# Kernel optimization log

Hardware: AMD Instinct MI355X
Metric: run time of the kernel (lower is better)

Reference implementation:

```python
import jax, jax.numpy as jnp
import numpy as np

H = 512          # hidden_dim
T = 20           # output_seq_len
EPS = 1e-5


def _ln(x, g, b):
    m = jnp.mean(x, axis=-1, keepdims=True)
    v = jnp.mean((x - m) ** 2, axis=-1, keepdims=True)
    return (x - m) * jax.lax.rsqrt(v + EPS) * g + b


def setup_inputs() -> dict:
    key = jax.random.key(0)
    ks = jax.random.split(key, 20)
    N, LD, PD = 65536, 128, 32
    s = 0.02
    return {
        "z_q": jax.random.normal(ks[0], (N, LD), jnp.float32),
        "f_prior": jax.random.normal(ks[1], (N, PD), jnp.float32),
        # init_mlp: Linear(160 -> 1024) -> LN -> GELU -> Linear(1024 -> 512) -> Tanh
        "W1": jax.random.normal(ks[2], (LD + PD, 2 * H), jnp.float32) * s,
        "b1": jnp.zeros((2 * H,), jnp.float32),
        "g1": jnp.ones((2 * H,), jnp.float32),
        "be1": jnp.zeros((2 * H,), jnp.float32),
        "W2": jax.random.normal(ks[3], (2 * H, H), jnp.float32) * s,
        "b2": jnp.zeros((H,), jnp.float32),
        # start token (output_dim = 1)
        "start_token": jax.random.normal(ks[4], (1,), jnp.float32) * 0.1,
        # GRU, input_size=1, hidden_size=H, gates stacked [r, z, n] (torch layout)
        "W_ih": jax.random.normal(ks[5], (3 * H, 1), jnp.float32) * s,
        "W_hh": jax.random.normal(ks[6], (3 * H, H), jnp.float32) * s,
        "b_ih": jnp.zeros((3 * H,), jnp.float32),
        "b_hh": jnp.zeros((3 * H,), jnp.float32),
        # output_mlp: Linear(H -> H//2) -> LN -> GELU -> Linear(H//2 -> 1)
        "Wo1": jax.random.normal(ks[7], (H, H // 2), jnp.float32) * s,
        "bo1": jnp.zeros((H // 2,), jnp.float32),
        "go": jnp.ones((H // 2,), jnp.float32),
        "beo": jnp.zeros((H // 2,), jnp.float32),
        "Wo2": jax.random.normal(ks[8], (H // 2, 1), jnp.float32) * s,
        "bo2": jnp.zeros((1,), jnp.float32),
    }


def reference(z_q, f_prior, W1, b1, g1, be1, W2, b2, start_token,
              W_ih, W_hh, b_ih, b_hh, Wo1, bo1, go, beo, Wo2, bo2):
    N = z_q.shape[0]
    # init_mlp -> h_0 (dropout is identity at eval)
    combined = jnp.concatenate([z_q, f_prior], axis=1)          # (N, LD+PD)
    h = jnp.tanh(jax.nn.gelu(_ln(combined @ W1 + b1, g1, be1), approximate=False) @ W2 + b2)  # (N, H)

    x0 = jnp.broadcast_to(start_token[None, :], (N, 1))          # (N, 1)

    def step(carry, _):
        h, x = carry
        gi = x @ W_ih.T + b_ih                                   # (N, 3H)
        gh = h @ W_hh.T + b_hh                                   # (N, 3H)
        r = jax.nn.sigmoid(gi[:, :H] + gh[:, :H])
        z = jax.nn.sigmoid(gi[:, H:2 * H] + gh[:, H:2 * H])
        n = jnp.tanh(gi[:, 2 * H:] + r * gh[:, 2 * H:])
        h_new = (1.0 - z) * n + z * h
        y = jax.nn.gelu(_ln(h_new @ Wo1 + bo1, go, beo), approximate=False) @ Wo2 + bo2  # (N, 1)
        return (h_new, y), y

    _, ys = jax.lax.scan(step, (h, x0), None, length=T)          # (T, N, 1)
    preds = jnp.transpose(ys[..., 0], (1, 0))                    # (N, T), output_dim==1 squeeze
    return preds
```

## Files before the change

kernel.cpp:

```cpp
#include <hip/hip_runtime.h>
#include <math.h>


typedef _Float16 f16;
typedef _Float16 f16x4 __attribute__((ext_vector_type(4)));
typedef _Float16 f16x8 __attribute__((ext_vector_type(8)));
typedef float f32x4 __attribute__((ext_vector_type(4)));

#define TSTEPS 20

__device__ __forceinline__ float sigm(float v) { return 1.0f / (1.0f + __expf(-v)); }
__device__ __forceinline__ float tanh_s(float v) {
  float e = __expf(-2.0f * fabsf(v));
  float r = (1.0f - e) / (1.0f + e);
  return copysignf(r, v);
}
__device__ __forceinline__ float gelu_e(float v) {
  return 0.5f * v * (1.0f + erff(v * 0.70710678118654752f));
}
__device__ __forceinline__ void st4(float* d, float4 v) {
  d[0] = v.x; d[1] = v.y; d[2] = v.z; d[3] = v.w;
}

__device__ __forceinline__ int haddr(int buf, int m, int k) {
  return buf + m * 1024 + ((k * 2) ^ ((m & 7) << 4));
}
__device__ __forceinline__ int taddr(int m, int c) {
  return m * 2048 + ((c * 2) ^ ((m & 7) << 4));
}

__global__ void cvt_weights(const float* __restrict__ W1, const float* __restrict__ W2,
                            const float* __restrict__ Whh, const float* __restrict__ Wo1,
                            f16* __restrict__ w1t, f16* __restrict__ w2t,
                            f16* __restrict__ whh, f16* __restrict__ wo1t) {
  int i = blockIdx.x * 256 + threadIdx.x;
  if (i < 163840) { int n = i / 160; int k = i - n * 160; w1t[i] = (f16)W1[k * 1024 + n]; return; }
  i -= 163840;
  if (i < 524288) { int n = i >> 10; int k = i & 1023; w2t[i] = (f16)W2[k * 512 + n]; return; }
  i -= 524288;
  if (i < 786432) { whh[i] = (f16)Whh[i]; return; }
  i -= 786432;
  if (i < 131072) { int o = i >> 9; int k = i & 511; wo1t[i] = (f16)Wo1[k * 256 + o]; return; }
}

__global__ __launch_bounds__(512) __attribute__((amdgpu_waves_per_eu(2, 2)))
void gru_main(
    const float* __restrict__ zq, const float* __restrict__ fpr,
    const float* __restrict__ b1, const float* __restrict__ g1, const float* __restrict__ be1,
    const float* __restrict__ b2, const float* __restrict__ stok,
    const float* __restrict__ Wih, const float* __restrict__ bih, const float* __restrict__ bhh,
    const float* __restrict__ bo1, const float* __restrict__ go, const float* __restrict__ beo,
    const float* __restrict__ Wo2, const float* __restrict__ bo2,
    const f16* __restrict__ w1t, const f16* __restrict__ w2t,
    const f16* __restrict__ whh, const f16* __restrict__ wo1t,
    float* __restrict__ out) {
  __shared__ __align__(16) unsigned char sm[131072];
  __shared__ float sm_stat[64 * 9 * 2];
  __shared__ float sm_yp[64 * 9];
  __shared__ float sm_x[64];

  const int tid = threadIdx.x;
  const int w = tid >> 6;
  const int lane = tid & 63;
  const int l16 = lane & 15;
  const int l4 = lane >> 4;
  const int R0 = blockIdx.x * 64;

  if (tid < 64) sm_x[tid] = stok[0];

  #pragma unroll 1
  for (int p = 0; p < 4; ++p) {
    f32x4 acc[4][2];
    #pragma unroll
    for (int mt = 0; mt < 4; ++mt)
      #pragma unroll
      for (int jh = 0; jh < 2; ++jh) acc[mt][jh] = (f32x4){0.f, 0.f, 0.f, 0.f};
    #pragma unroll
    for (int kf = 0; kf < 5; ++kf) {
      const int k0 = kf * 32 + l4 * 8;
      f16x8 B[4];
      #pragma unroll
      for (int mt = 0; mt < 4; ++mt) {
        const int gm = R0 + mt * 16 + l16;
        const float* src = (kf < 4) ? (zq + gm * 128 + k0) : (fpr + gm * 32 + (k0 - 128));
        float4 v0 = *(const float4*)src;
        float4 v1 = *(const float4*)(src + 4);
        f16x8 b;
        b[0] = (f16)v0.x; b[1] = (f16)v0.y; b[2] = (f16)v0.z; b[3] = (f16)v0.w;
        b[4] = (f16)v1.x; b[5] = (f16)v1.y; b[6] = (f16)v1.z; b[7] = (f16)v1.w;
        B[mt] = b;
      }
      f16x8 A[2];
      #pragma unroll
      for (int jh = 0; jh < 2; ++jh)
        A[jh] = *(const f16x8*)(w1t + (w * 128 + (p * 2 + jh) * 16 + l16) * 160 + k0);
      #pragma unroll
      for (int mt = 0; mt < 4; ++mt)
        #pragma unroll
        for (int jh = 0; jh < 2; ++jh)
          acc[mt][jh] = __builtin_amdgcn_mfma_f32_16x16x32_f16(A[jh], B[mt], acc[mt][jh], 0, 0, 0);
    }
    #pragma unroll
    for (int jh = 0; jh < 2; ++jh) {
      const int jq = w * 128 + (p * 2 + jh) * 16 + l4 * 4;
      const float4 bb = *(const float4*)(b1 + jq);
      float bbv[4]; st4(bbv, bb);
      #pragma unroll
      for (int mt = 0; mt < 4; ++mt) {
        const int m = mt * 16 + l16;
        f16x4 v;
        #pragma unroll
        for (int r = 0; r < 4; ++r) v[r] = (f16)(acc[mt][jh][r] + bbv[r]);
        *(f16x4*)(sm + taddr(m, jq)) = v;
      }
    }
  }
  __syncthreads();
  {
    const int m = lane;
    float s = 0.f, ss = 0.f;
    #pragma unroll 4
    for (int cb = 0; cb < 16; ++cb) {
      const int c = w * 128 + cb * 8;
      f16x8 v = *(const f16x8*)(sm + taddr(m, c));
      #pragma unroll
      for (int i = 0; i < 8; ++i) { float f = (float)v[i]; s += f; ss += f * f; }
    }
    sm_stat[(m * 9 + w) * 2] = s;
    sm_stat[(m * 9 + w) * 2 + 1] = ss;
    __syncthreads();
    s = 0.f; ss = 0.f;
    #pragma unroll
    for (int i = 0; i < 8; ++i) { s += sm_stat[(m * 9 + i) * 2]; ss += sm_stat[(m * 9 + i) * 2 + 1]; }
    const float mean = s * (1.f / 1024.f);
    const float rstd = rsqrtf(ss * (1.f / 1024.f) - mean * mean + 1e-5f);
    #pragma unroll 2
    for (int cb = 0; cb < 16; ++cb) {
      const int c = w * 128 + cb * 8;
      f16x8 v = *(const f16x8*)(sm + taddr(m, c));
      float4 ga = *(const float4*)(g1 + c);
      float4 gb = *(const float4*)(g1 + c + 4);
      float4 ba = *(const float4*)(be1 + c);
      float4 bb = *(const float4*)(be1 + c + 4);
      float gs[8] = {ga.x, ga.y, ga.z, ga.w, gb.x, gb.y, gb.z, gb.w};
      float bs[8] = {ba.x, ba.y, ba.z, ba.w, bb.x, bb.y, bb.z, bb.w};
      f16x8 o;
      #pragma unroll
      for (int i = 0; i < 8; ++i)
        o[i] = (f16)gelu_e(((float)v[i] - mean) * rstd * gs[i] + bs[i]);
      *(f16x8*)(sm + taddr(m, c)) = o;
    }
  }
  __syncthreads();
  f16x4 hold[2][4][2];
  #pragma unroll
  for (int p = 0; p < 2; ++p) {
    f32x4 acc[4][2];
    #pragma unroll
    for (int mt = 0; mt < 4; ++mt)
      #pragma unroll
      for (int jh = 0; jh < 2; ++jh) acc[mt][jh] = (f32x4){0.f, 0.f, 0.f, 0.f};
    #pragma unroll 4
    for (int kf = 0; kf < 32; ++kf) {
      const int k0 = kf * 32 + l4 * 8;
      f16x8 B[4];
      #pragma unroll
      for (int mt = 0; mt < 4; ++mt)
        B[mt] = *(const f16x8*)(sm + taddr(mt * 16 + l16, k0));
      f16x8 A[2];
      #pragma unroll
      for (int jh = 0; jh < 2; ++jh)
        A[jh] = *(const f16x8*)(w2t + (w * 64 + (p * 2 + jh) * 16 + l16) * 1024 + k0);
      #pragma unroll
      for (int mt = 0; mt < 4; ++mt)
        #pragma unroll
        for (int jh = 0; jh < 2; ++jh)
          acc[mt][jh] = __builtin_amdgcn_mfma_f32_16x16x32_f16(A[jh], B[mt], acc[mt][jh], 0, 0, 0);
    }
    #pragma unroll
    for (int jh = 0; jh < 2; ++jh) {
      const int jq = w * 64 + (p * 2 + jh) * 16 + l4 * 4;
      const float4 bb = *(const float4*)(b2 + jq);
      float bbv[4]; st4(bbv, bb);
      #pragma unroll
      for (int mt = 0; mt < 4; ++mt) {
        f16x4 v;
        #pragma unroll
        for (int r = 0; r < 4; ++r) v[r] = (f16)tanh_s(acc[mt][jh][r] + bbv[r]);
        hold[p][mt][jh] = v;
      }
    }
  }
  __syncthreads();
  #pragma unroll
  for (int p = 0; p < 2; ++p)
    #pragma unroll
    for (int jh = 0; jh < 2; ++jh) {
      const int jq = w * 64 + (p * 2 + jh) * 16 + l4 * 4;
      #pragma unroll
      for (int mt = 0; mt < 4; ++mt) {
        const int m = mt * 16 + l16;
        *(f16x4*)(sm + haddr(0, m, jq)) = hold[p][mt][jh];
      }
    }
  __syncthreads();

  #pragma unroll 1
  for (int t = 0; t < TSTEPS; ++t) {
    const int cur = (t & 1) << 16;
    const int nxt = cur ^ 65536;
    #pragma unroll 1
    for (int p = 0; p < 2; ++p) {
      f32x4 acc[4][3][2];
      #pragma unroll
      for (int mt = 0; mt < 4; ++mt)
        #pragma unroll
        for (int g = 0; g < 3; ++g)
          #pragma unroll
          for (int jh = 0; jh < 2; ++jh) acc[mt][g][jh] = (f32x4){0.f, 0.f, 0.f, 0.f};
      #pragma unroll 4
      for (int kf = 0; kf < 16; ++kf) {
        const int k0 = kf * 32 + l4 * 8;
        f16x8 B[4];
        #pragma unroll
        for (int mt = 0; mt < 4; ++mt)
          B[mt] = *(const f16x8*)(sm + haddr(cur, mt * 16 + l16, k0));
        f16x8 A[3][2];
        #pragma unroll
        for (int g = 0; g < 3; ++g)
          #pragma unroll
          for (int jh = 0; jh < 2; ++jh)
            A[g][jh] = *(const f16x8*)(whh + (g * 512 + w * 64 + (p * 2 + jh) * 16 + l16) * 512 + k0);
        #pragma unroll
        for (int mt = 0; mt < 4; ++mt)
          #pragma unroll
          for (int g = 0; g < 3; ++g)
            #pragma unroll
            for (int jh = 0; jh < 2; ++jh)
              acc[mt][g][jh] = __builtin_amdgcn_mfma_f32_16x16x32_f16(A[g][jh], B[mt], acc[mt][g][jh], 0, 0, 0);
      }
      #pragma unroll
      for (int jh = 0; jh < 2; ++jh) {
        const int jq = w * 64 + (p * 2 + jh) * 16 + l4 * 4;
        float wr[4], wz[4], wn[4], br[4], bz[4], bn[4], cr[4], cz[4], cn[4];
        st4(wr, *(const float4*)(Wih + jq));
        st4(wz, *(const float4*)(Wih + 512 + jq));
        st4(wn, *(const float4*)(Wih + 1024 + jq));
        st4(br, *(const float4*)(bih + jq));
        st4(bz, *(const float4*)(bih + 512 + jq));
        st4(bn, *(const float4*)(bih + 1024 + jq));
        st4(cr, *(const float4*)(bhh + jq));
        st4(cz, *(const float4*)(bhh + 512 + jq));
        st4(cn, *(const float4*)(bhh + 1024 + jq));
        #pragma unroll
        for (int mt = 0; mt < 4; ++mt) {
          const int m = mt * 16 + l16;
          const float x = sm_x[m];
          const int hoff = m * 1024 + ((jq * 2) ^ ((m & 7) << 4));
          const f16x4 ho = *(const f16x4*)(sm + cur + hoff);
          f16x4 hn;
          #pragma unroll
          for (int r = 0; r < 4; ++r) {
            const float gr = sigm(x * wr[r] + br[r] + acc[mt][0][jh][r] + cr[r]);
            const float gz = sigm(x * wz[r] + bz[r] + acc[mt][1][jh][r] + cz[r]);
            const float gn = tanh_s(x * wn[r] + bn[r] + gr * (acc[mt][2][jh][r] + cn[r]));
            hn[r] = (f16)((1.f - gz) * gn + gz * (float)ho[r]);
          }
          *(f16x4*)(sm + nxt + hoff) = hn;
        }
      }
    }
    __syncthreads();
    {
      f32x4 a2[4][2];
      #pragma unroll
      for (int mt = 0; mt < 4; ++mt)
        #pragma unroll
        for (int jt = 0; jt < 2; ++jt) a2[mt][jt] = (f32x4){0.f, 0.f, 0.f, 0.f};
      #pragma unroll 4
      for (int kf = 0; kf < 16; ++kf) {
        const int k0 = kf * 32 + l4 * 8;
        f16x8 B[4];
        #pragma unroll
        for (int mt = 0; mt < 4; ++mt)
          B[mt] = *(const f16x8*)(sm + haddr(nxt, mt * 16 + l16, k0));
        f16x8 A[2];
        #pragma unroll
        for (int jt = 0; jt < 2; ++jt)
          A[jt] = *(const f16x8*)(wo1t + (w * 32 + jt * 16 + l16) * 512 + k0);
        #pragma unroll
        for (int mt = 0; mt < 4; ++mt)
          #pragma unroll
          for (int jt = 0; jt < 2; ++jt)
            a2[mt][jt] = __builtin_amdgcn_mfma_f32_16x16x32_f16(A[jt], B[mt], a2[mt][jt], 0, 0, 0);
      }
      float vv[4][2][4];
      float bo1v[2][4];
      #pragma unroll
      for (int jt = 0; jt < 2; ++jt)
        st4(bo1v[jt], *(const float4*)(bo1 + w * 32 + jt * 16 + l4 * 4));
      float sA[4], sB[4];
      #pragma unroll
      for (int mt = 0; mt < 4; ++mt) {
        float s = 0.f, ss = 0.f;
        #pragma unroll
        for (int jt = 0; jt < 2; ++jt)
          #pragma unroll
          for (int r = 0; r < 4; ++r) {
            const float v = a2[mt][jt][r] + bo1v[jt][r];
            vv[mt][jt][r] = v; s += v; ss += v * v;
          }
        s += __shfl_xor(s, 16); ss += __shfl_xor(ss, 16);
        s += __shfl_xor(s, 32); ss += __shfl_xor(ss, 32);
        sA[mt] = s; sB[mt] = ss;
      }
      if (l4 == 0) {
        #pragma unroll
        for (int mt = 0; mt < 4; ++mt) {
          const int m = mt * 16 + l16;
          sm_stat[(m * 9 + w) * 2] = sA[mt];
          sm_stat[(m * 9 + w) * 2 + 1] = sB[mt];
        }
      }
      __syncthreads();
      float gov[2][4], bev[2][4], wv[2][4];
      #pragma unroll
      for (int jt = 0; jt < 2; ++jt) {
        const int jb = w * 32 + jt * 16 + l4 * 4;
        st4(gov[jt], *(const float4*)(go + jb));
        st4(bev[jt], *(const float4*)(beo + jb));
        st4(wv[jt], *(const float4*)(Wo2 + jb));
      }
      float yp[4];
      #pragma unroll
      for (int mt = 0; mt < 4; ++mt) {
        const int m = mt * 16 + l16;
        float s = 0.f, ss = 0.f;
        #pragma unroll
        for (int i = 0; i < 8; ++i) {
          s += sm_stat[(m * 9 + i) * 2];
          ss += sm_stat[(m * 9 + i) * 2 + 1];
        }
        const float mean = s * (1.f / 256.f);
        const float rstd = rsqrtf(ss * (1.f / 256.f) - mean * mean + 1e-5f);
        float y = 0.f;
        #pragma unroll
        for (int jt = 0; jt < 2; ++jt)
          #pragma unroll
          for (int r = 0; r < 4; ++r)
            y += gelu_e((vv[mt][jt][r] - mean) * rstd * gov[jt][r] + bev[jt][r]) * wv[jt][r];
        y += __shfl_xor(y, 16);
        y += __shfl_xor(y, 32);
        yp[mt] = y;
      }
      if (l4 == 0) {
        #pragma unroll
        for (int mt = 0; mt < 4; ++mt)
          sm_yp[(mt * 16 + l16) * 9 + w] = yp[mt];
      }
      __syncthreads();
      if (w == 0 && l4 == 0) {
        #pragma unroll
        for (int mt = 0; mt < 4; ++mt) {
          const int m = mt * 16 + l16;
          float y = bo2[0];
          #pragma unroll
          for (int i = 0; i < 8; ++i) y += sm_yp[m * 9 + i];
          sm_x[m] = y;
          out[(R0 + m) * 20 + t] = y;
        }
      }
      __syncthreads();
    }
  }
}

extern "C" void kernel_launch(void* const* d_in, const int* in_sizes, int n_in,
                              void* d_out, int out_size, void* d_ws, size_t ws_size,
                              hipStream_t stream) {
  const float* zq   = (const float*)d_in[0];
  const float* fpr  = (const float*)d_in[1];
  const float* W1   = (const float*)d_in[2];
  const float* b1   = (const float*)d_in[3];
  const float* g1   = (const float*)d_in[4];
  const float* be1  = (const float*)d_in[5];
  const float* W2   = (const float*)d_in[6];
  const float* b2   = (const float*)d_in[7];
  const float* stok = (const float*)d_in[8];
  const float* Wih  = (const float*)d_in[9];
  const float* Whh  = (const float*)d_in[10];
  const float* bih  = (const float*)d_in[11];
  const float* bhh  = (const float*)d_in[12];
  const float* Wo1  = (const float*)d_in[13];
  const float* bo1  = (const float*)d_in[14];
  const float* go   = (const float*)d_in[15];
  const float* beo  = (const float*)d_in[16];
  const float* Wo2  = (const float*)d_in[17];
  const float* bo2  = (const float*)d_in[18];

  char* ws = (char*)d_ws;
  f16* w1t  = (f16*)(ws + 0);
  f16* w2t  = (f16*)(ws + 327680);
  f16* whh  = (f16*)(ws + 1376256);
  f16* wo1t = (f16*)(ws + 2949120);

  cvt_weights<<<6272, 256, 0, stream>>>(W1, W2, Whh, Wo1, w1t, w2t, whh, wo1t);

  const int N = in_sizes[0] / 128;
  gru_main<<<N / 64, 512, 0, stream>>>(zq, fpr, b1, g1, be1, b2, stok, Wih, bih, bhh,
                                       bo1, go, beo, Wo2, bo2, w1t, w2t, whh, wo1t,
                                       (float*)d_out);
}
```

Before: 5.299 ms.

## Halve LDS and registers to allow two blocks per CU

LDS drops from 128KB to 64KB. The hidden-state double buffer becomes a single buffer, with new h values held in registers until a barrier and then written back. The init MLP now runs in two 32-row halves so its pre-activation tile fits the smaller buffer. Per-iteration accumulator sets are smaller, waves_per_eu rises to 4, and the final per-row output sum is computed redundantly by every wave, which removes one barrier and the sm_x buffer. This aims for higher occupancy so latency is hidden better, at the cost of an extra barrier per step and possible register spills.

```diff
diff --git a/kernel.cpp b/kernel.cpp
--- a/kernel.cpp
+++ b/kernel.cpp
@@ -22,8 +22,8 @@
   d[0] = v.x; d[1] = v.y; d[2] = v.z; d[3] = v.w;
 }
 
-__device__ __forceinline__ int haddr(int buf, int m, int k) {
-  return buf + m * 1024 + ((k * 2) ^ ((m & 7) << 4));
+__device__ __forceinline__ int haddr(int m, int k) {
+  return m * 1024 + ((k * 2) ^ ((m & 7) << 4));
 }
 __device__ __forceinline__ int taddr(int m, int c) {
   return m * 2048 + ((c * 2) ^ ((m & 7) << 4));
@@ -43,7 +43,7 @@
   if (i < 131072) { int o = i >> 9; int k = i & 511; wo1t[i] = (f16)Wo1[k * 256 + o]; return; }
 }
 
-__global__ __launch_bounds__(512) __attribute__((amdgpu_waves_per_eu(2, 2)))
+__global__ __launch_bounds__(512) __attribute__((amdgpu_waves_per_eu(4)))
 void gru_main(
     const float* __restrict__ zq, const float* __restrict__ fpr,
     const float* __restrict__ b1, const float* __restrict__ g1, const float* __restrict__ be1,
@@ -54,10 +54,9 @@
     const f16* __restrict__ w1t, const f16* __restrict__ w2t,
     const f16* __restrict__ whh, const f16* __restrict__ wo1t,
     float* __restrict__ out) {
-  __shared__ __align__(16) unsigned char sm[131072];
+  __shared__ __align__(16) unsigned char sm[65536];
   __shared__ float sm_stat[64 * 9 * 2];
   __shared__ float sm_yp[64 * 9];
-  __shared__ float sm_x[64];
 
   const int tid = threadIdx.x;
   const int w = tid >> 6;
@@ -66,209 +65,207 @@
   const int l4 = lane >> 4;
   const int R0 = blockIdx.x * 64;
 
-  if (tid < 64) sm_x[tid] = stok[0];
+  const float bo2v = bo2[0];
+  float x4[4];
+  {
+    const float s0 = stok[0];
+    #pragma unroll
+    for (int mt = 0; mt < 4; ++mt) x4[mt] = s0;
+  }
+
+  f16x4 h0h[2][2][2][2];
 
   #pragma unroll 1
-  for (int p = 0; p < 4; ++p) {
-    f32x4 acc[4][2];
+  for (int hh = 0; hh < 2; ++hh) {
+    const int RH = R0 + hh * 32;
+    #pragma unroll 1
+    for (int q = 0; q < 4; ++q) {
+      f32x4 acc[2][2];
+      #pragma unroll
+      for (int mt = 0; mt < 2; ++mt)
+        #pragma unroll
+        for (int jh = 0; jh < 2; ++jh) acc[mt][jh] = (f32x4){0.f, 0.f, 0.f, 0.f};
+      #pragma unroll
+      for (int kf = 0; kf < 5; ++kf) {
+        const int k0 = kf * 32 + l4 * 8;
+        f16x8 B[2];
+        #pragma unroll
+        for (int mt = 0; mt < 2; ++mt) {
+          const int gm = RH + mt * 16 + l16;
+          const float* src = (kf < 4) ? (zq + gm * 128 + k0) : (fpr + gm * 32 + (k0 - 128));
+          float4 v0 = *(const float4*)src;
+          float4 v1 = *(const float4*)(src + 4);
+          f16x8 b;
+          b[0] = (f16)v0.x; b[1] = (f16)v0.y; b[2] = (f16)v0.z; b[3] = (f16)v0.w;
+          b[4] = (f16)v1.x; b[5] = (f16)v1.y; b[6] = (f16)v1.z; b[7] = (f16)v1.w;
+          B[mt] = b;
+        }
+        #pragma unroll
+        for (int jh = 0; jh < 2; ++jh) {
+          const f16x8 A = *(const f16x8*)(w1t + (w * 128 + q * 32 + jh * 16 + l16) * 160 + k0);
+          #pragma unroll
+          for (int mt = 0; mt < 2; ++mt)
+            acc[mt][jh] = __builtin_amdgcn_mfma_f32_16x16x32_f16(A, B[mt], acc[mt][jh], 0, 0, 0);
+        }
+      }
+      #pragma unroll
+      for (int jh = 0; jh < 2; ++jh) {
+        const int jq = w * 128 + q * 32 + jh * 16 + l4 * 4;
+        float bb[4]; st4(bb, *(const float4*)(b1 + jq));
+        #pragma unroll
+        for (int mt = 0; mt < 2; ++mt) {
+          f16x4 v;
+          #pragma unroll
+          for (int r = 0; r < 4; ++r) v[r] = (f16)(acc[mt][jh][r] + bb[r]);
+          *(f16x4*)(sm + taddr(mt * 16 + l16, jq)) = v;
+        }
+      }
+    }
+    __syncthreads();
+    {
+      const int m = tid >> 4;
+      const int c0 = (tid & 15) * 64;
+      float s = 0.f, ss = 0.f;
+      #pragma unroll
+      for (int cb = 0; cb < 8; ++cb) {
+        f16x8 v = *(const f16x8*)(sm + taddr(m, c0 + cb * 8));
+        #pragma unroll
+        for (int i = 0; i < 8; ++i) { float f = (float)v[i]; s += f; ss += f * f; }
+      }
+      s += __shfl_xor(s, 1); ss += __shfl_xor(ss, 1);
+      s += __shfl_xor(s, 2); ss += __shfl_xor(ss, 2);
+      s += __shfl_xor(s, 4); ss += __shfl_xor(ss, 4);
+      s += __shfl_xor(s, 8); ss += __shfl_xor(ss, 8);
+      const float mean = s * (1.f / 1024.f);
+      const float rstd = rsqrtf(ss * (1.f / 1024.f) - mean * mean + 1e-5f);
+      #pragma unroll 2
+      for (int cb = 0; cb < 8; ++cb) {
+        const int c = c0 + cb * 8;
+        f16x8 v = *(const f16x8*)(sm + taddr(m, c));
+        float4 ga = *(const float4*)(g1 + c);
+        float4 gb = *(const float4*)(g1 + c + 4);
+        float4 ba = *(const float4*)(be1 + c);
+        float4 bb = *(const float4*)(be1 + c + 4);
+        float gs[8] = {ga.x, ga.y, ga.z, ga.w, gb.x, gb.y, gb.z, gb.w};
+        float bs[8] = {ba.x, ba.y, ba.z, ba.w, bb.x, bb.y, bb.z, bb.w};
+        f16x8 o;
+        #pragma unroll
+        for (int i = 0; i < 8; ++i)
+          o[i] = (f16)gelu_e(((float)v[i] - mean) * rstd * gs[i] + bs[i]);
+        *(f16x8*)(sm + taddr(m, c)) = o;
+      }
+    }
+    __syncthreads();
+    #pragma unroll 1
+    for (int p = 0; p < 2; ++p) {
+      f32x4 acc[2][2];
+      #pragma unroll
+      for (int mt = 0; mt < 2; ++mt)
+        #pragma unroll
+        for (int jh = 0; jh < 2; ++jh) acc[mt][jh] = (f32x4){0.f, 0.f, 0.f, 0.f};
+      #pragma unroll 2
+      for (int kf = 0; kf < 32; ++kf) {
+        const int k0 = kf * 32 + l4 * 8;
+        f16x8 B[2];
+        #pragma unroll
+        for (int mt = 0; mt < 2; ++mt)
+          B[mt] = *(const f16x8*)(sm + taddr(mt * 16 + l16, k0));
+        #pragma unroll
+        for (int jh = 0; jh < 2; ++jh) {
+          const f16x8 A = *(const f16x8*)(w2t + (w * 64 + p * 32 + jh * 16 + l16) * 1024 + k0);
+          #pragma unroll
+          for (int mt = 0; mt < 2; ++mt)
+            acc[mt][jh] = __builtin_amdgcn_mfma_f32_16x16x32_f16(A, B[mt], acc[mt][jh], 0, 0, 0);
+        }
+      }
+      #pragma unroll
+      for (int jh = 0; jh < 2; ++jh) {
+        const int jq = w * 64 + p * 32 + jh * 16 + l4 * 4;
+        float bb[4]; st4(bb, *(const float4*)(b2 + jq));
+        #pragma unroll
+        for (int mt = 0; mt < 2; ++mt) {
+          f16x4 v;
+          #pragma unroll
+          for (int r = 0; r < 4; ++r) v[r] = (f16)tanh_s(acc[mt][jh][r] + bb[r]);
+          h0h[hh][p][jh][mt] = v;
+        }
+      }
+    }
+    __syncthreads();
+  }
+  #pragma unroll
+  for (int hh = 0; hh < 2; ++hh)
     #pragma unroll
-    for (int mt = 0; mt < 4; ++mt)
-      #pragma unroll
-      for (int jh = 0; jh < 2; ++jh) acc[mt][jh] = (f32x4){0.f, 0.f, 0.f, 0.f};
-    #pragma unroll
-    for (int kf = 0; kf < 5; ++kf) {
-      const int k0 = kf * 32 + l4 * 8;
-      f16x8 B[4];
-      #pragma unroll
-      for (int mt = 0; mt < 4; ++mt) {
-        const int gm = R0 + mt * 16 + l16;
-        const float* src = (kf < 4) ? (zq + gm * 128 + k0) : (fpr + gm * 32 + (k0 - 128));
-        float4 v0 = *(const float4*)src;
-        float4 v1 = *(const float4*)(src + 4);
-        f16x8 b;
-        b[0] = (f16)v0.x; b[1] = (f16)v0.y; b[2] = (f16)v0.z; b[3] = (f16)v0.w;
-        b[4] = (f16)v1.x; b[5] = (f16)v1.y; b[6] = (f16)v1.z; b[7] = (f16)v1.w;
-        B[mt] = b;
-      }
-      f16x8 A[2];
-      #pragma unroll
-      for (int jh = 0; jh < 2; ++jh)
-        A[jh] = *(const f16x8*)(w1t + (w * 128 + (p * 2 + jh) * 16 + l16) * 160 + k0);
-      #pragma unroll
-      for (int mt = 0; mt < 4; ++mt)
-        #pragma unroll
-        for (int jh = 0; jh < 2; ++jh)
-          acc[mt][jh] = __builtin_amdgcn_mfma_f32_16x16x32_f16(A[jh], B[mt], acc[mt][jh], 0, 0, 0);
-    }
-    #pragma unroll
-    for (int jh = 0; jh < 2; ++jh) {
-      const int jq = w * 128 + (p * 2 + jh) * 16 + l4 * 4;
-      const float4 bb = *(const float4*)(b1 + jq);
-      float bbv[4]; st4(bbv, bb);
-      #pragma unroll
-      for (int mt = 0; mt < 4; ++mt) {
-        const int m = mt * 16 + l16;
-        f16x4 v;
-        #pragma unroll
-        for (int r = 0; r < 4; ++r) v[r] = (f16)(acc[mt][jh][r] + bbv[r]);
-        *(f16x4*)(sm + taddr(m, jq)) = v;
-      }
-    }
-  }
-  __syncthreads();
-  {
-    const int m = lane;
-    float s = 0.f, ss = 0.f;
-    #pragma unroll 4
-    for (int cb = 0; cb < 16; ++cb) {
-      const int c = w * 128 + cb * 8;
-      f16x8 v = *(const f16x8*)(sm + taddr(m, c));
-      #pragma unroll
-      for (int i = 0; i < 8; ++i) { float f = (float)v[i]; s += f; ss += f * f; }
-    }
-    sm_stat[(m * 9 + w) * 2] = s;
-    sm_stat[(m * 9 + w) * 2 + 1] = ss;
-    __syncthreads();
-    s = 0.f; ss = 0.f;
-    #pragma unroll
-    for (int i = 0; i < 8; ++i) { s += sm_stat[(m * 9 + i) * 2]; ss += sm_stat[(m * 9 + i) * 2 + 1]; }
-    const float mean = s * (1.f / 1024.f);
-    const float rstd = rsqrtf(ss * (1.f / 1024.f) - mean * mean + 1e-5f);
-    #pragma unroll 2
-    for (int cb = 0; cb < 16; ++cb) {
-      const int c = w * 128 + cb * 8;
-      f16x8 v = *(const f16x8*)(sm + taddr(m, c));
-      float4 ga = *(const float4*)(g1 + c);
-      float4 gb = *(const float4*)(g1 + c + 4);
-      float4 ba = *(const float4*)(be1 + c);
-      float4 bb = *(const float4*)(be1 + c + 4);
-      float gs[8] = {ga.x, ga.y, ga.z, ga.w, gb.x, gb.y, gb.z, gb.w};
-      float bs[8] = {ba.x, ba.y, ba.z, ba.w, bb.x, bb.y, bb.z, bb.w};
-      f16x8 o;
-      #pragma unroll
-      for (int i = 0; i < 8; ++i)
-        o[i] = (f16)gelu_e(((float)v[i] - mean) * rstd * gs[i] + bs[i]);
-      *(f16x8*)(sm + taddr(m, c)) = o;
-    }
-  }
-  __syncthreads();
-  f16x4 hold[2][4][2];
-  #pragma unroll
-  for (int p = 0; p < 2; ++p) {
-    f32x4 acc[4][2];
-    #pragma unroll
-    for (int mt = 0; mt < 4; ++mt)
-      #pragma unroll
-      for (int jh = 0; jh < 2; ++jh) acc[mt][jh] = (f32x4){0.f, 0.f, 0.f, 0.f};
-    #pragma unroll 4
-    for (int kf = 0; kf < 32; ++kf) {
-      const int k0 = kf * 32 + l4 * 8;
-      f16x8 B[4];
-      #pragma unroll
-      for (int mt = 0; mt < 4; ++mt)
-        B[mt] = *(const f16x8*)(sm + taddr(mt * 16 + l16, k0));
-      f16x8 A[2];
-      #pragma unroll
-      for (int jh = 0; jh < 2; ++jh)
-        A[jh] = *(const f16x8*)(w2t + (w * 64 + (p * 2 + jh) * 16 + l16) * 1024 + k0);
-      #pragma unroll
-      for (int mt = 0; mt < 4; ++mt)
-        #pragma unroll
-        for (int jh = 0; jh < 2; ++jh)
-          acc[mt][jh] = __builtin_amdgcn_mfma_f32_16x16x32_f16(A[jh], B[mt], acc[mt][jh], 0, 0, 0);
-    }
-    #pragma unroll
-    for (int jh = 0; jh < 2; ++jh) {
-      const int jq = w * 64 + (p * 2 + jh) * 16 + l4 * 4;
-      const float4 bb = *(const float4*)(b2 + jq);
-      float bbv[4]; st4(bbv, bb);
-      #pragma unroll
-      for (int mt = 0; mt < 4; ++mt) {
-        f16x4 v;
-        #pragma unroll
-        for (int r = 0; r < 4; ++r) v[r] = (f16)tanh_s(acc[mt][jh][r] + bbv[r]);
-        hold[p][mt][jh] = v;
-      }
-    }
-  }
-  __syncthreads();
-  #pragma unroll
-  for (int p = 0; p < 2; ++p)
-    #pragma unroll
-    for (int jh = 0; jh < 2; ++jh) {
-      const int jq = w * 64 + (p * 2 + jh) * 16 + l4 * 4;
-      #pragma unroll
-      for (int mt = 0; mt < 4; ++mt) {
-        const int m = mt * 16 + l16;
-        *(f16x4*)(sm + haddr(0, m, jq)) = hold[p][mt][jh];
-      }
-    }
+    for (int p = 0; p < 2; ++p)
+      #pragma unroll
+      for (int jh = 0; jh < 2; ++jh) {
+        const int k = w * 64 + p * 32 + jh * 16 + l4 * 4;
+        #pragma unroll
+        for (int mt = 0; mt < 2; ++mt)
+          *(f16x4*)(sm + haddr(hh * 32 + mt * 16 + l16, k)) = h0h[hh][p][jh][mt];
+      }
   __syncthreads();
 
   #pragma unroll 1
   for (int t = 0; t < TSTEPS; ++t) {
-    const int cur = (t & 1) << 16;
-    const int nxt = cur ^ 65536;
+    f16x4 hnh[4][4];
     #pragma unroll 1
-    for (int p = 0; p < 2; ++p) {
-      f32x4 acc[4][3][2];
+    for (int q = 0; q < 4; ++q) {
+      const int jt = w * 64 + q * 16;
+      f32x4 acc[4][3];
       #pragma unroll
       for (int mt = 0; mt < 4; ++mt)
         #pragma unroll
-        for (int g = 0; g < 3; ++g)
-          #pragma unroll
-          for (int jh = 0; jh < 2; ++jh) acc[mt][g][jh] = (f32x4){0.f, 0.f, 0.f, 0.f};
-      #pragma unroll 4
+        for (int g = 0; g < 3; ++g) acc[mt][g] = (f32x4){0.f, 0.f, 0.f, 0.f};
+      #pragma unroll 2
       for (int kf = 0; kf < 16; ++kf) {
         const int k0 = kf * 32 + l4 * 8;
         f16x8 B[4];
         #pragma unroll
         for (int mt = 0; mt < 4; ++mt)
-          B[mt] = *(const f16x8*)(sm + haddr(cur, mt * 16 + l16, k0));
-        f16x8 A[3][2];
-        #pragma unroll
-        for (int g = 0; g < 3; ++g)
-          #pragma unroll
-          for (int jh = 0; jh < 2; ++jh)
-            A[g][jh] = *(const f16x8*)(whh + (g * 512 + w * 64 + (p * 2 + jh) * 16 + l16) * 512 + k0);
-        #pragma unroll
-        for (int mt = 0; mt < 4; ++mt)
-          #pragma unroll
-          for (int g = 0; g < 3; ++g)
-            #pragma unroll
-            for (int jh = 0; jh < 2; ++jh)
-              acc[mt][g][jh] = __builtin_amdgcn_mfma_f32_16x16x32_f16(A[g][jh], B[mt], acc[mt][g][jh], 0, 0, 0);
-      }
-      #pragma unroll
-      for (int jh = 0; jh < 2; ++jh) {
-        const int jq = w * 64 + (p * 2 + jh) * 16 + l4 * 4;
-        float wr[4], wz[4], wn[4], br[4], bz[4], bn[4], cr[4], cz[4], cn[4];
-        st4(wr, *(const float4*)(Wih + jq));
-        st4(wz, *(const float4*)(Wih + 512 + jq));
-        st4(wn, *(const float4*)(Wih + 1024 + jq));
-        st4(br, *(const float4*)(bih + jq));
-        st4(bz, *(const float4*)(bih + 512 + jq));
-        st4(bn, *(const float4*)(bih + 1024 + jq));
-        st4(cr, *(const float4*)(bhh + jq));
-        st4(cz, *(const float4*)(bhh + 512 + jq));
-        st4(cn, *(const float4*)(bhh + 1024 + jq));
-        #pragma unroll
-        for (int mt = 0; mt < 4; ++mt) {
-          const int m = mt * 16 + l16;
-          const float x = sm_x[m];
-          const int hoff = m * 1024 + ((jq * 2) ^ ((m & 7) << 4));
-          const f16x4 ho = *(const f16x4*)(sm + cur + hoff);
-          f16x4 hn;
-          #pragma unroll
-          for (int r = 0; r < 4; ++r) {
-            const float gr = sigm(x * wr[r] + br[r] + acc[mt][0][jh][r] + cr[r]);
-            const float gz = sigm(x * wz[r] + bz[r] + acc[mt][1][jh][r] + cz[r]);
-            const float gn = tanh_s(x * wn[r] + bn[r] + gr * (acc[mt][2][jh][r] + cn[r]));
-            hn[r] = (f16)((1.f - gz) * gn + gz * (float)ho[r]);
-          }
-          *(f16x4*)(sm + nxt + hoff) = hn;
-        }
-      }
+          B[mt] = *(const f16x8*)(sm + haddr(mt * 16 + l16, k0));
+        #pragma unroll
+        for (int g = 0; g < 3; ++g) {
+          const f16x8 A = *(const f16x8*)(whh + (g * 512 + jt + l16) * 512 + k0);
+          #pragma unroll
+          for (int mt = 0; mt < 4; ++mt)
+            acc[mt][g] = __builtin_amdgcn_mfma_f32_16x16x32_f16(A, B[mt], acc[mt][g], 0, 0, 0);
+        }
+      }
+      const int jq = jt + l4 * 4;
+      float wr[4], wz[4], wn[4], br[4], bz[4], bn[4], cr[4], cz[4], cn[4];
+      st4(wr, *(const float4*)(Wih + jq));
+      st4(wz, *(const float4*)(Wih + 512 + jq));
+      st4(wn, *(const float4*)(Wih + 1024 + jq));
+      st4(br, *(const float4*)(bih + jq));
+      st4(bz, *(const float4*)(bih + 512 + jq));
+      st4(bn, *(const float4*)(bih + 1024 + jq));
+      st4(cr, *(const float4*)(bhh + jq));
+      st4(cz, *(const float4*)(bhh + 512 + jq));
+      st4(cn, *(const float4*)(bhh + 1024 + jq));
+      #pragma unroll
+      for (int mt = 0; mt < 4; ++mt) {
+        const int m = mt * 16 + l16;
+        const float x = x4[mt];
+        const f16x4 ho = *(const f16x4*)(sm + haddr(m, jq));
+        f16x4 hn;
+        #pragma unroll
+        for (int r = 0; r < 4; ++r) {
+          const float gr = sigm(x * wr[r] + br[r] + acc[mt][0][r] + cr[r]);
+          const float gz = sigm(x * wz[r] + bz[r] + acc[mt][1][r] + cz[r]);
+          const float gn = tanh_s(x * wn[r] + bn[r] + gr * (acc[mt][2][r] + cn[r]));
+          hn[r] = (f16)((1.f - gz) * gn + gz * (float)ho[r]);
+        }
+        hnh[q][mt] = hn;
+      }
+    }
+    __syncthreads();
+    #pragma unroll
+    for (int q = 0; q < 4; ++q) {
+      const int jq = w * 64 + q * 16 + l4 * 4;
+      #pragma unroll
+      for (int mt = 0; mt < 4; ++mt)
+        *(f16x4*)(sm + haddr(mt * 16 + l16, jq)) = hnh[q][mt];
     }
     __syncthreads();
     {
@@ -276,62 +273,54 @@
       #pragma unroll
       for (int mt = 0; mt < 4; ++mt)
         #pragma unroll
-        for (int jt = 0; jt < 2; ++jt) a2[mt][jt] = (f32x4){0.f, 0.f, 0.f, 0.f};
-      #pragma unroll 4
+        for (int jt2 = 0; jt2 < 2; ++jt2) a2[mt][jt2] = (f32x4){0.f, 0.f, 0.f, 0.f};
+      #pragma unroll 2
       for (int kf = 0; kf < 16; ++kf) {
         const int k0 = kf * 32 + l4 * 8;
         f16x8 B[4];
         #pragma unroll
         for (int mt = 0; mt < 4; ++mt)
-          B[mt] = *(const f16x8*)(sm + haddr(nxt, mt * 16 + l16, k0));
-        f16x8 A[2];
-        #pragma unroll
-        for (int jt = 0; jt < 2; ++jt)
-          A[jt] = *(const f16x8*)(wo1t + (w * 32 + jt * 16 + l16) * 512 + k0);
-        #pragma unroll
-        for (int mt = 0; mt < 4; ++mt)
-          #pragma unroll
-          for (int jt = 0; jt < 2; ++jt)
-            a2[mt][jt] = __builtin_amdgcn_mfma_f32_16x16x32_f16(A[jt], B[mt], a2[mt][jt], 0, 0, 0);
+          B[mt] = *(const f16x8*)(sm + haddr(mt * 16 + l16, k0));
+        #pragma unroll
+        for (int jt2 = 0; jt2 < 2; ++jt2) {
+          const f16x8 A = *(const f16x8*)(wo1t + (w * 32 + jt2 * 16 + l16) * 512 + k0);
+          #pragma unroll
+          for (int mt = 0; mt < 4; ++mt)
+            a2[mt][jt2] = __builtin_amdgcn_mfma_f32_16x16x32_f16(A, B[mt], a2[mt][jt2], 0, 0, 0);
+        }
       }
       float vv[4][2][4];
       float bo1v[2][4];
       #pragma unroll
-      for (int jt = 0; jt < 2; ++jt)
-        st4(bo1v[jt], *(const float4*)(bo1 + w * 32 + jt * 16 + l4 * 4));
-      float sA[4], sB[4];
+      for (int jt2 = 0; jt2 < 2; ++jt2)
+        st4(bo1v[jt2], *(const float4*)(bo1 + w * 32 + jt2 * 16 + l4 * 4));
       #pragma unroll
       for (int mt = 0; mt < 4; ++mt) {
         float s = 0.f, ss = 0.f;
         #pragma unroll
-        for (int jt = 0; jt < 2; ++jt)
+        for (int jt2 = 0; jt2 < 2; ++jt2)
           #pragma unroll
           for (int r = 0; r < 4; ++r) {
-            const float v = a2[mt][jt][r] + bo1v[jt][r];
-            vv[mt][jt][r] = v; s += v; ss += v * v;
+            const float v = a2[mt][jt2][r] + bo1v[jt2][r];
+            vv[mt][jt2][r] = v; s += v; ss += v * v;
           }
         s += __shfl_xor(s, 16); ss += __shfl_xor(ss, 16);
         s += __shfl_xor(s, 32); ss += __shfl_xor(ss, 32);
-        sA[mt] = s; sB[mt] = ss;
-      }
-      if (l4 == 0) {
-        #pragma unroll
-        for (int mt = 0; mt < 4; ++mt) {
+        if (l4 == 0) {
           const int m = mt * 16 + l16;
-          sm_stat[(m * 9 + w) * 2] = sA[mt];
-          sm_stat[(m * 9 + w) * 2 + 1] = sB[mt];
+          sm_stat[(m * 9 + w) * 2] = s;
+          sm_stat[(m * 9 + w) * 2 + 1] = ss;
         }
       }
       __syncthreads();
       float gov[2][4], bev[2][4], wv[2][4];
       #pragma unroll
-      for (int jt = 0; jt < 2; ++jt) {
-        const int jb = w * 32 + jt * 16 + l4 * 4;
-        st4(gov[jt], *(const float4*)(go + jb));
-        st4(bev[jt], *(const float4*)(beo + jb));
-        st4(wv[jt], *(const float4*)(Wo2 + jb));
-      }
-      float yp[4];
+      for (int jt2 = 0; jt2 < 2; ++jt2) {
+        const int jb = w * 32 + jt2 * 16 + l4 * 4;
+        st4(gov[jt2], *(const float4*)(go + jb));
+        st4(bev[jt2], *(const float4*)(beo + jb));
+        st4(wv[jt2], *(const float4*)(Wo2 + jb));
+      }
       #pragma unroll
       for (int mt = 0; mt < 4; ++mt) {
         const int m = mt * 16 + l16;
@@ -345,32 +334,24 @@
         const float rstd = rsqrtf(ss * (1.f / 256.f) - mean * mean + 1e-5f);
         float y = 0.f;
         #pragma unroll
-        for (int jt = 0; jt < 2; ++jt)
+        for (int jt2 = 0; jt2 < 2; ++jt2)
           #pragma unroll
           for (int r = 0; r < 4; ++r)
-            y += gelu_e((vv[mt][jt][r] - mean) * rstd * gov[jt][r] + bev[jt][r]) * wv[jt][r];
+            y += gelu_e((vv[mt][jt2][r] - mean) * rstd * gov[jt2][r] + bev[jt2][r]) * wv[jt2][r];
         y += __shfl_xor(y, 16);
         y += __shfl_xor(y, 32);
-        yp[mt] = y;
-      }
-      if (l4 == 0) {
-        #pragma unroll
-        for (int mt = 0; mt < 4; ++mt)
-          sm_yp[(mt * 16 + l16) * 9 + w] = yp[mt];
+        if (l4 == 0) sm_yp[m * 9 + w] = y;
       }
       __syncthreads();
-      if (w == 0 && l4 == 0) {
-        #pragma unroll
-        for (int mt = 0; mt < 4; ++mt) {
-          const int m = mt * 16 + l16;
-          float y = bo2[0];
-          #pragma unroll
-          for (int i = 0; i < 8; ++i) y += sm_yp[m * 9 + i];
-          sm_x[m] = y;
-          out[(R0 + m) * 20 + t] = y;
-        }
-      }
-      __syncthreads();
+      #pragma unroll
+      for (int mt = 0; mt < 4; ++mt) {
+        const int m = mt * 16 + l16;
+        float ys = bo2v;
+        #pragma unroll
+        for (int i = 0; i < 8; ++i) ys += sm_yp[m * 9 + i];
+        x4[mt] = ys;
+        if (w == 0 && l4 == 0) out[(R0 + m) * 20 + t] = ys;
+      }
     }
   }
 }
```

After: 8.629 ms. 62.8% more time.
